# Kernel optimization log

Measured on AMD Instinct MI355X. Metric: run time of the kernel, lower is better.

Reference implementation:

```python
import jax, jax.numpy as jnp
import numpy as np

B, S, D, H = 2, 2048, 1024, 16
DH = D // H  # 64
SCALE = DH ** -0.5


def setup_inputs() -> dict:
    key = jax.random.key(0)
    ks = jax.random.split(key, 6)
    std = D ** -0.5
    return {
        "Q": jax.random.normal(ks[0], (B, S, D), jnp.float32),
        "prev": jax.random.normal(ks[1], (B, H, S, S), jnp.float32),
        "W_qkv": jax.random.normal(ks[2], (D, 3 * D), jnp.float32) * std,
        "b_qkv": jax.random.normal(ks[3], (3 * D,), jnp.float32) * 0.01,
        "W_out": jax.random.normal(ks[4], (D, D), jnp.float32) * std,
        "b_out": jax.random.normal(ks[5], (D,), jnp.float32) * 0.01,
    }


def reference(Q, prev, W_qkv, b_qkv, W_out, b_out):
    # fused QKV projection: [B,S,3D]
    qkv = jnp.einsum("bsd,de->bse", Q, W_qkv) + b_qkv
    # [B,S,H,3*DH] then split into q,k,v each [B,S,H,DH]
    qkv = qkv.reshape(B, S, H, 3 * DH)
    q, k, v = jnp.split(qkv, 3, axis=-1)
    # scores [B,H,S,S] with residual attention add
    scores = jnp.einsum("bqhd,bkhd->bhqk", q, k) * SCALE + prev
    attn = jax.nn.softmax(scores, axis=-1)  # dropout p=0.0 -> identity
    # context [B,S,H,DH] -> [B,S,D]
    context = jnp.einsum("bhqk,bkhd->bqhd", attn, v).reshape(B, S, D)
    output = jnp.einsum("bsd,de->bse", context, W_out) + b_out
    return output, scores
```

## Files before the change

kernel.cpp:

```cpp
#include <hip/hip_runtime.h>

typedef __attribute__((ext_vector_type(8))) short bf16x8;
typedef __attribute__((ext_vector_type(4))) float f32x4;
typedef __attribute__((ext_vector_type(4))) unsigned short u16x4;
typedef unsigned short ushort_t;
typedef unsigned int uint32;

constexpr int B_ = 2, S_ = 2048, D_ = 1024, H_ = 16, DH_ = 64;
constexpr int M_TOK = B_ * S_;
constexpr int N_QKV = 3 * D_;

#define DEV __device__ __forceinline__

DEV ushort_t f2bf(float f) {
  uint32 u = __builtin_bit_cast(uint32, f);
  u += 0x7fffu + ((u >> 16) & 1u);
  return (ushort_t)(u >> 16);
}

DEV float bf2f(ushort_t u) {
  uint32 x = ((uint32)u) << 16;
  return __builtin_bit_cast(float, x);
}

DEV void gll16(const void* g, void* l) {
  __builtin_amdgcn_global_load_lds(
      (const __attribute__((address_space(1))) void*)g,
      (__attribute__((address_space(3))) void*)l, 16, 0, 0);
}

__global__ __launch_bounds__(256) void k_cvt_q(const float* __restrict__ in,
                                               ushort_t* __restrict__ out) {
  int i = (blockIdx.x * 256 + threadIdx.x) * 4;
  float4 v = *(const float4*)(in + i);
  u16x4 o;
  o.x = f2bf(v.x); o.y = f2bf(v.y); o.z = f2bf(v.z); o.w = f2bf(v.w);
  *(u16x4*)(out + i) = o;
}

__global__ __launch_bounds__(256) void k_transpose_cvt(const float* __restrict__ in,
                                                       ushort_t* __restrict__ out,
                                                       int R, int C) {
  __shared__ float t[32][33];
  int bx = blockIdx.x, by = blockIdx.y;
  int tx = threadIdx.x & 31, ty = threadIdx.x >> 5;
#pragma unroll
  for (int i = 0; i < 4; ++i) {
    int r = by * 32 + ty + i * 8;
    t[ty + i * 8][tx] = in[(size_t)r * C + bx * 32 + tx];
  }
  __syncthreads();
#pragma unroll
  for (int i = 0; i < 4; ++i) {
    int orow = bx * 32 + ty + i * 8;
    int ocol = by * 32 + tx;
    out[(size_t)orow * R + ocol] = f2bf(t[tx][ty + i * 8]);
  }
}

__global__ __launch_bounds__(256) void k_gemm_qkv(
    const ushort_t* __restrict__ A,
    const ushort_t* __restrict__ Bt,
    const float* __restrict__ bias,
    ushort_t* __restrict__ qh,
    ushort_t* __restrict__ kh,
    ushort_t* __restrict__ vT) {
  constexpr int K = 1024;
  __shared__ ushort_t lA[128 * 32];
  __shared__ ushort_t lB[128 * 32];
  const int t = threadIdx.x, lane = t & 63, w = t >> 6;
  const int wm = w >> 1, wn = w & 1;
  const int bm = blockIdx.x & 31, bn = blockIdx.x >> 5;

  f32x4 acc[4][4];
#pragma unroll
  for (int i = 0; i < 4; ++i)
#pragma unroll
    for (int j = 0; j < 4; ++j) acc[i][j] = f32x4{0.f, 0.f, 0.f, 0.f};

  const int srow = t >> 2;
  const int scol = (t & 3) * 8;
  for (int k0 = 0; k0 < K; k0 += 32) {
    __syncthreads();
    gll16(A + (size_t)(bm * 128 + srow) * K + k0 + scol, lA + srow * 32 + scol);
    gll16(A + (size_t)(bm * 128 + 64 + srow) * K + k0 + scol, lA + (64 + srow) * 32 + scol);
    gll16(Bt + (size_t)(bn * 128 + srow) * K + k0 + scol, lB + srow * 32 + scol);
    gll16(Bt + (size_t)(bn * 128 + 64 + srow) * K + k0 + scol, lB + (64 + srow) * 32 + scol);
    asm volatile("s_waitcnt vmcnt(0)" ::: "memory");
    __syncthreads();
    bf16x8 af[4], bfr[4];
#pragma unroll
    for (int i = 0; i < 4; ++i)
      af[i] = *(const bf16x8*)(lA + (wm * 64 + i * 16 + (lane & 15)) * 32 + (lane >> 4) * 8);
#pragma unroll
    for (int j = 0; j < 4; ++j)
      bfr[j] = *(const bf16x8*)(lB + (wn * 64 + j * 16 + (lane & 15)) * 32 + (lane >> 4) * 8);
#pragma unroll
    for (int i = 0; i < 4; ++i)
#pragma unroll
      for (int j = 0; j < 4; ++j)
        acc[i][j] = __builtin_amdgcn_mfma_f32_16x16x32_bf16(af[i], bfr[j], acc[i][j], 0, 0, 0);
  }
#pragma unroll
  for (int i = 0; i < 4; ++i) {
#pragma unroll
    for (int j = 0; j < 4; ++j) {
#pragma unroll
      for (int p = 0; p < 4; ++p) {
        int row = bm * 128 + wm * 64 + i * 16 + (lane >> 4) * 4 + p;
        int col = bn * 128 + wn * 64 + j * 16 + (lane & 15);
        float v = acc[i][j][p] + bias[col];
        ushort_t bv = f2bf(v);
        int b = row >> 11, s = row & (S_ - 1);
        int h = col / 192, r = col - h * 192;
        size_t bh = (size_t)(b * H_ + h);
        if (r < 64)
          qh[(bh * S_ + s) * 64 + r] = bv;
        else if (r < 128)
          kh[(bh * S_ + s) * 64 + (r - 64)] = bv;
        else
          vT[(bh * 64 + (r - 128)) * S_ + s] = bv;
      }
    }
  }
}

__global__ __launch_bounds__(256, 2) void k_scores_pv(
    const ushort_t* __restrict__ qhp,
    const ushort_t* __restrict__ khp,
    const ushort_t* __restrict__ vT,
    const float* __restrict__ prev,
    float* __restrict__ scores,
    float* __restrict__ pstats,
    ushort_t* __restrict__ Opart) {
  __shared__ ushort_t lK[512 * 64];
  __shared__ ushort_t Plds[4][2048];
  const int t = threadIdx.x, lane = t & 63, w = t >> 6;
  int idx = (int)blockIdx.x;
  idx = (idx & 7) * 512 + (idx >> 3);
  const int rt = idx & 31, ct = (idx >> 5) & 3, bh = idx >> 7;
  const int row0 = rt * 64 + w * 16;
  const int kt0 = ct * 512;
  const int lo = lane & 15, hi = lane >> 4;

  const ushort_t* qb = qhp + ((size_t)bh * S_ + row0) * 64;
  const ushort_t* kb = khp + ((size_t)bh * S_ + kt0) * 64;
  const ushort_t* vb = vT + (size_t)bh * 64 * S_ + kt0;
  const float* pb = prev + (size_t)bh * S_ * S_ + (size_t)(row0 + lo) * S_ + kt0;
  float* sb = scores + (size_t)bh * S_ * S_ + (size_t)(row0 + lo) * S_ + kt0;

  bf16x8 qf0 = *(const bf16x8*)(qb + lo * 64 + hi * 8);
  bf16x8 qf1 = *(const bf16x8*)(qb + lo * 64 + 32 + hi * 8);

#pragma unroll
  for (int i = 0; i < 16; ++i) {
    int u = i * 256 + t;
    int r = u >> 3;
    int s = (u & 7) * 16;
    int cb = s ^ ((r & 7) << 4);
    gll16(kb + (size_t)r * 64 + cb / 2, (ushort_t*)lK + u * 8);
  }
  float4 pcur[8];
#pragma unroll
  for (int kf = 0; kf < 8; ++kf)
    pcur[kf] = *(const float4*)(pb + kf * 16 + hi * 4);
  asm volatile("s_waitcnt vmcnt(0)" ::: "memory");
  __syncthreads();

  const int swz = (lo & 7) << 4;
  const char* lkb = (const char*)lK;
  char* pw = (char*)&Plds[w][0];

  f32x4 acco[4];
#pragma unroll
  for (int dn = 0; dn < 4; ++dn) acco[dn] = f32x4{0.f, 0.f, 0.f, 0.f};
  float m_run = -1e30f, l_run = 0.f;

  for (int c = 0; c < 4; ++c) {
    bf16x8 vf[4][4];
#pragma unroll
    for (int kc = 0; kc < 4; ++kc)
#pragma unroll
      for (int dn = 0; dn < 4; ++dn)
        vf[kc][dn] = *(const bf16x8*)(vb + (size_t)(dn * 16 + lo) * S_ +
                                      c * 128 + kc * 32 + hi * 8);
    float4 pnext[8];
    if (c < 3) {
#pragma unroll
      for (int kf = 0; kf < 8; ++kf)
        pnext[kf] = *(const float4*)(pb + (c + 1) * 128 + kf * 16 + hi * 4);
    }
    f32x4 acc[8];
#pragma unroll
    for (int kf = 0; kf < 8; ++kf) acc[kf] = f32x4{0.f, 0.f, 0.f, 0.f};
#pragma unroll
    for (int kf = 0; kf < 8; ++kf) {
      int krow = c * 128 + kf * 16 + lo;
      bf16x8 k0 = *(const bf16x8*)(lkb + krow * 128 + ((hi * 16) ^ swz));
      bf16x8 k1 = *(const bf16x8*)(lkb + krow * 128 + ((64 + hi * 16) ^ swz));
      acc[kf] = __builtin_amdgcn_mfma_f32_16x16x32_bf16(k0, qf0, acc[kf], 0, 0, 0);
      acc[kf] = __builtin_amdgcn_mfma_f32_16x16x32_bf16(k1, qf1, acc[kf], 0, 0, 0);
    }
    float tmax = -1e30f;
#pragma unroll
    for (int kf = 0; kf < 8; ++kf) {
      acc[kf][0] = acc[kf][0] * 0.125f + pcur[kf].x;
      acc[kf][1] = acc[kf][1] * 0.125f + pcur[kf].y;
      acc[kf][2] = acc[kf][2] * 0.125f + pcur[kf].z;
      acc[kf][3] = acc[kf][3] * 0.125f + pcur[kf].w;
      __builtin_nontemporal_store(acc[kf], (f32x4*)(sb + c * 128 + kf * 16 + hi * 4));
      tmax = fmaxf(tmax, fmaxf(fmaxf(acc[kf][0], acc[kf][1]), fmaxf(acc[kf][2], acc[kf][3])));
    }
    tmax = fmaxf(tmax, __shfl_xor(tmax, 16));
    tmax = fmaxf(tmax, __shfl_xor(tmax, 32));
    float m_new = fmaxf(m_run, tmax);
    float fs = __expf(m_run - m_new);
    float lsum = 0.f;
#pragma unroll
    for (int kf = 0; kf < 8; ++kf) {
      float e0 = __expf(acc[kf][0] - m_new);
      float e1 = __expf(acc[kf][1] - m_new);
      float e2 = __expf(acc[kf][2] - m_new);
      float e3 = __expf(acc[kf][3] - m_new);
      lsum += (e0 + e1) + (e2 + e3);
      u16x4 pk;
      pk.x = f2bf(e0); pk.y = f2bf(e1); pk.z = f2bf(e2); pk.w = f2bf(e3);
      int byte = (lo * 256 + kf * 32 + hi * 8) ^ swz;
      *(u16x4*)(pw + byte) = pk;
    }
    lsum += __shfl_xor(lsum, 16);
    lsum += __shfl_xor(lsum, 32);
    m_run = m_new;
    l_run = l_run * fs + lsum;
#pragma unroll
    for (int dn = 0; dn < 4; ++dn)
#pragma unroll
      for (int p = 0; p < 4; ++p) acco[dn][p] *= fs;
#pragma unroll
    for (int kc = 0; kc < 4; ++kc) {
      int byte = (lo * 256 + kc * 64 + hi * 16) ^ swz;
      bf16x8 pa = *(const bf16x8*)(pw + byte);
#pragma unroll
      for (int dn = 0; dn < 4; ++dn)
        acco[dn] = __builtin_amdgcn_mfma_f32_16x16x32_bf16(vf[kc][dn], pa, acco[dn], 0, 0, 0);
    }
    if (c < 3) {
#pragma unroll
      for (int kf = 0; kf < 8; ++kf) pcur[kf] = pnext[kf];
    }
  }
  ushort_t* ob = Opart + (((size_t)bh * S_ + row0 + lo) * 4 + ct) * 64;
#pragma unroll
  for (int dn = 0; dn < 4; ++dn) {
    u16x4 ov;
#pragma unroll
    for (int p = 0; p < 4; ++p) ov[p] = f2bf(acco[dn][p]);
    *(u16x4*)(ob + dn * 16 + hi * 4) = ov;
  }
  if (hi == 0)
    *(float2*)(pstats + (((size_t)bh * S_ + row0 + lo) * 4 + ct) * 2) =
        float2{m_run, l_run};
}

__global__ __launch_bounds__(256) void k_combine(
    const float* __restrict__ pstats,
    const ushort_t* __restrict__ Opart,
    ushort_t* __restrict__ ctx) {
  const int t = threadIdx.x;
  const int row = blockIdx.x * 64 + (t >> 2);
  const int hi4 = t & 3;
  const int bh = row >> 11, s = row & (S_ - 1);

  const float* ps = pstats + (size_t)row * 8;
  float2 st[4];
#pragma unroll
  for (int i = 0; i < 4; ++i) st[i] = *(const float2*)(ps + i * 2);
  float m = fmaxf(fmaxf(st[0].x, st[1].x), fmaxf(st[2].x, st[3].x));
  float den = 0.f;
#pragma unroll
  for (int i = 0; i < 4; ++i) den += st[i].y * __expf(st[i].x - m);
  float sc[4];
#pragma unroll
  for (int i = 0; i < 4; ++i) sc[i] = __expf(st[i].x - m) / den;

  const ushort_t* ob = Opart + (size_t)row * 256 + hi4 * 16;
  float o[16];
#pragma unroll
  for (int j = 0; j < 16; ++j) o[j] = 0.f;
#pragma unroll
  for (int i = 0; i < 4; ++i) {
    bf16x8 a0 = *(const bf16x8*)(ob + i * 64);
    bf16x8 a1 = *(const bf16x8*)(ob + i * 64 + 8);
#pragma unroll
    for (int j = 0; j < 8; ++j) {
      o[j]     += bf2f((ushort_t)a0[j]) * sc[i];
      o[8 + j] += bf2f((ushort_t)a1[j]) * sc[i];
    }
  }
  const int b = bh >> 4, h = bh & 15;
  ushort_t* cp = ctx + (size_t)(b * S_ + s) * D_ + h * 64 + hi4 * 16;
#pragma unroll
  for (int g = 0; g < 4; ++g) {
    u16x4 ov;
#pragma unroll
    for (int p = 0; p < 4; ++p) ov[p] = f2bf(o[g * 4 + p]);
    *(u16x4*)(cp + g * 4) = ov;
  }
}

__global__ __launch_bounds__(256) void k_gemm_out(
    const ushort_t* __restrict__ A,
    const ushort_t* __restrict__ Bt,
    const float* __restrict__ bias,
    float* __restrict__ out) {
  constexpr int K = 1024;
  __shared__ ushort_t lA[128 * 32];
  __shared__ ushort_t lB[128 * 32];
  const int t = threadIdx.x, lane = t & 63, w = t >> 6;
  const int wm = w >> 1, wn = w & 1;
  const int bm = blockIdx.x & 31, bn = blockIdx.x >> 5;

  f32x4 acc[4][4];
#pragma unroll
  for (int i = 0; i < 4; ++i)
#pragma unroll
    for (int j = 0; j < 4; ++j) acc[i][j] = f32x4{0.f, 0.f, 0.f, 0.f};

  const int srow = t >> 2;
  const int scol = (t & 3) * 8;
  for (int k0 = 0; k0 < K; k0 += 32) {
    __syncthreads();
    gll16(A + (size_t)(bm * 128 + srow) * K + k0 + scol, lA + srow * 32 + scol);
    gll16(A + (size_t)(bm * 128 + 64 + srow) * K + k0 + scol, lA + (64 + srow) * 32 + scol);
    gll16(Bt + (size_t)(bn * 128 + srow) * K + k0 + scol, lB + srow * 32 + scol);
    gll16(Bt + (size_t)(bn * 128 + 64 + srow) * K + k0 + scol, lB + (64 + srow) * 32 + scol);
    asm volatile("s_waitcnt vmcnt(0)" ::: "memory");
    __syncthreads();
    bf16x8 af[4], bfr[4];
#pragma unroll
    for (int i = 0; i < 4; ++i)
      af[i] = *(const bf16x8*)(lA + (wm * 64 + i * 16 + (lane & 15)) * 32 + (lane >> 4) * 8);
#pragma unroll
    for (int j = 0; j < 4; ++j)
      bfr[j] = *(const bf16x8*)(lB + (wn * 64 + j * 16 + (lane & 15)) * 32 + (lane >> 4) * 8);
#pragma unroll
    for (int i = 0; i < 4; ++i)
#pragma unroll
      for (int j = 0; j < 4; ++j)
        acc[i][j] = __builtin_amdgcn_mfma_f32_16x16x32_bf16(af[i], bfr[j], acc[i][j], 0, 0, 0);
  }
#pragma unroll
  for (int i = 0; i < 4; ++i) {
#pragma unroll
    for (int j = 0; j < 4; ++j) {
#pragma unroll
      for (int p = 0; p < 4; ++p) {
        int row = bm * 128 + wm * 64 + i * 16 + (lane >> 4) * 4 + p;
        int col = bn * 128 + wn * 64 + j * 16 + (lane & 15);
        out[(size_t)row * 1024 + col] = acc[i][j][p] + bias[col];
      }
    }
  }
}

extern "C" void kernel_launch(void* const* d_in, const int* in_sizes, int n_in,
                              void* d_out, int out_size, void* d_ws, size_t ws_size,
                              hipStream_t stream) {
  (void)in_sizes; (void)n_in; (void)out_size; (void)ws_size;
  const float* Q     = (const float*)d_in[0];
  const float* prev  = (const float*)d_in[1];
  const float* W_qkv = (const float*)d_in[2];
  const float* b_qkv = (const float*)d_in[3];
  const float* W_out = (const float*)d_in[4];
  const float* b_out = (const float*)d_in[5];
  float* out = (float*)d_out;
  float* scores_out = out + (size_t)M_TOK * D_;

  char* ws = (char*)d_ws;
  ushort_t* Qb    = (ushort_t*)(ws + (size_t)0);
  ushort_t* WqkvT = (ushort_t*)(ws + ((size_t)8  << 20));
  ushort_t* WoutT = (ushort_t*)(ws + ((size_t)14 << 20));
  ushort_t* qh    = (ushort_t*)(ws + ((size_t)16 << 20));
  ushort_t* kh    = (ushort_t*)(ws + ((size_t)24 << 20));
  ushort_t* vT    = (ushort_t*)(ws + ((size_t)32 << 20));
  ushort_t* ctx   = (ushort_t*)(ws + ((size_t)40 << 20));
  ushort_t* Opart = (ushort_t*)(ws + ((size_t)48 << 20));
  float*    pstats = (float*)Qb;

  k_cvt_q<<<4096, 256, 0, stream>>>(Q, Qb);
  k_transpose_cvt<<<dim3(96, 32), 256, 0, stream>>>(W_qkv, WqkvT, 1024, 3072);
  k_transpose_cvt<<<dim3(32, 32), 256, 0, stream>>>(W_out, WoutT, 1024, 1024);
  k_gemm_qkv<<<768, 256, 0, stream>>>(Qb, WqkvT, b_qkv, qh, kh, vT);
  k_scores_pv<<<4096, 256, 0, stream>>>(qh, kh, vT, prev, scores_out, pstats, Opart);
  k_combine<<<1024, 256, 0, stream>>>(pstats, Opart, ctx);
  k_gemm_out<<<256, 256, 0, stream>>>(ctx, WoutT, b_out, out);
}
```

Measured before the change: 423.9 us.

## Make scores kernel persistent over eight row tiles to reuse LDS K tile

Each block of the scores/PV kernel now handles eight consecutive 64-row tiles for one (head, 512-column) slice instead of one, so the K slice staged in LDS is reused eight times and the grid drops from 4096 to 512 blocks. The next tile's Q fragments and first prev chunk are prefetched during the last chunk of the current tile through ping-ponged registers. The scores store changes from nontemporal to a plain store. The cost is fewer blocks (512 on a large GPU with two blocks per CU allowed), so latency hiding and load balance may suffer, and register pressure rises.

```diff
diff --git a/kernel.cpp b/kernel.cpp
--- a/kernel.cpp
+++ b/kernel.cpp
@@ -137,20 +137,16 @@
   __shared__ ushort_t Plds[4][2048];
   const int t = threadIdx.x, lane = t & 63, w = t >> 6;
   int idx = (int)blockIdx.x;
-  idx = (idx & 7) * 512 + (idx >> 3);
-  const int rt = idx & 31, ct = (idx >> 5) & 3, bh = idx >> 7;
-  const int row0 = rt * 64 + w * 16;
+  idx = (idx & 7) * 64 + (idx >> 3);
+  const int bh = idx >> 4, ct = (idx >> 2) & 3, rtg = idx & 3;
   const int kt0 = ct * 512;
   const int lo = lane & 15, hi = lane >> 4;
 
-  const ushort_t* qb = qhp + ((size_t)bh * S_ + row0) * 64;
+  const ushort_t* qbase = qhp + (size_t)bh * S_ * 64;
   const ushort_t* kb = khp + ((size_t)bh * S_ + kt0) * 64;
   const ushort_t* vb = vT + (size_t)bh * 64 * S_ + kt0;
-  const float* pb = prev + (size_t)bh * S_ * S_ + (size_t)(row0 + lo) * S_ + kt0;
-  float* sb = scores + (size_t)bh * S_ * S_ + (size_t)(row0 + lo) * S_ + kt0;
-
-  bf16x8 qf0 = *(const bf16x8*)(qb + lo * 64 + hi * 8);
-  bf16x8 qf1 = *(const bf16x8*)(qb + lo * 64 + 32 + hi * 8);
+  const float* prev_base = prev + (size_t)bh * S_ * S_ + kt0;
+  float* scores_base = scores + (size_t)bh * S_ * S_ + kt0;
 
 #pragma unroll
   for (int i = 0; i < 16; ++i) {
@@ -160,10 +156,14 @@
     int cb = s ^ ((r & 7) << 4);
     gll16(kb + (size_t)r * 64 + cb / 2, (ushort_t*)lK + u * 8);
   }
+  const int row00 = rtg * 512 + w * 16;
+  bf16x8 qfA0 = *(const bf16x8*)(qbase + (row00 + lo) * 64 + hi * 8);
+  bf16x8 qfA1 = *(const bf16x8*)(qbase + (row00 + lo) * 64 + 32 + hi * 8);
+  bf16x8 qfB0, qfB1;
   float4 pcur[8];
 #pragma unroll
   for (int kf = 0; kf < 8; ++kf)
-    pcur[kf] = *(const float4*)(pb + kf * 16 + hi * 4);
+    pcur[kf] = *(const float4*)(prev_base + (size_t)(row00 + lo) * S_ + kf * 16 + hi * 4);
   asm volatile("s_waitcnt vmcnt(0)" ::: "memory");
   __syncthreads();
 
@@ -171,95 +171,105 @@
   const char* lkb = (const char*)lK;
   char* pw = (char*)&Plds[w][0];
 
-  f32x4 acco[4];
-#pragma unroll
-  for (int dn = 0; dn < 4; ++dn) acco[dn] = f32x4{0.f, 0.f, 0.f, 0.f};
-  float m_run = -1e30f, l_run = 0.f;
-
-  for (int c = 0; c < 4; ++c) {
-    bf16x8 vf[4][4];
-#pragma unroll
-    for (int kc = 0; kc < 4; ++kc)
-#pragma unroll
-      for (int dn = 0; dn < 4; ++dn)
-        vf[kc][dn] = *(const bf16x8*)(vb + (size_t)(dn * 16 + lo) * S_ +
-                                      c * 128 + kc * 32 + hi * 8);
-    float4 pnext[8];
-    if (c < 3) {
-#pragma unroll
-      for (int kf = 0; kf < 8; ++kf)
-        pnext[kf] = *(const float4*)(pb + (c + 1) * 128 + kf * 16 + hi * 4);
-    }
-    f32x4 acc[8];
-#pragma unroll
-    for (int kf = 0; kf < 8; ++kf) acc[kf] = f32x4{0.f, 0.f, 0.f, 0.f};
-#pragma unroll
-    for (int kf = 0; kf < 8; ++kf) {
-      int krow = c * 128 + kf * 16 + lo;
-      bf16x8 k0 = *(const bf16x8*)(lkb + krow * 128 + ((hi * 16) ^ swz));
-      bf16x8 k1 = *(const bf16x8*)(lkb + krow * 128 + ((64 + hi * 16) ^ swz));
-      acc[kf] = __builtin_amdgcn_mfma_f32_16x16x32_bf16(k0, qf0, acc[kf], 0, 0, 0);
-      acc[kf] = __builtin_amdgcn_mfma_f32_16x16x32_bf16(k1, qf1, acc[kf], 0, 0, 0);
-    }
-    float tmax = -1e30f;
-#pragma unroll
-    for (int kf = 0; kf < 8; ++kf) {
-      acc[kf][0] = acc[kf][0] * 0.125f + pcur[kf].x;
-      acc[kf][1] = acc[kf][1] * 0.125f + pcur[kf].y;
-      acc[kf][2] = acc[kf][2] * 0.125f + pcur[kf].z;
-      acc[kf][3] = acc[kf][3] * 0.125f + pcur[kf].w;
-      __builtin_nontemporal_store(acc[kf], (f32x4*)(sb + c * 128 + kf * 16 + hi * 4));
-      tmax = fmaxf(tmax, fmaxf(fmaxf(acc[kf][0], acc[kf][1]), fmaxf(acc[kf][2], acc[kf][3])));
-    }
-    tmax = fmaxf(tmax, __shfl_xor(tmax, 16));
-    tmax = fmaxf(tmax, __shfl_xor(tmax, 32));
-    float m_new = fmaxf(m_run, tmax);
-    float fs = __expf(m_run - m_new);
-    float lsum = 0.f;
-#pragma unroll
-    for (int kf = 0; kf < 8; ++kf) {
-      float e0 = __expf(acc[kf][0] - m_new);
-      float e1 = __expf(acc[kf][1] - m_new);
-      float e2 = __expf(acc[kf][2] - m_new);
-      float e3 = __expf(acc[kf][3] - m_new);
-      lsum += (e0 + e1) + (e2 + e3);
-      u16x4 pk;
-      pk.x = f2bf(e0); pk.y = f2bf(e1); pk.z = f2bf(e2); pk.w = f2bf(e3);
-      int byte = (lo * 256 + kf * 32 + hi * 8) ^ swz;
-      *(u16x4*)(pw + byte) = pk;
-    }
-    lsum += __shfl_xor(lsum, 16);
-    lsum += __shfl_xor(lsum, 32);
-    m_run = m_new;
-    l_run = l_run * fs + lsum;
-#pragma unroll
-    for (int dn = 0; dn < 4; ++dn)
-#pragma unroll
-      for (int p = 0; p < 4; ++p) acco[dn][p] *= fs;
-#pragma unroll
-    for (int kc = 0; kc < 4; ++kc) {
-      int byte = (lo * 256 + kc * 64 + hi * 16) ^ swz;
-      bf16x8 pa = *(const bf16x8*)(pw + byte);
-#pragma unroll
-      for (int dn = 0; dn < 4; ++dn)
-        acco[dn] = __builtin_amdgcn_mfma_f32_16x16x32_bf16(vf[kc][dn], pa, acco[dn], 0, 0, 0);
-    }
-    if (c < 3) {
-#pragma unroll
-      for (int kf = 0; kf < 8; ++kf) pcur[kf] = pnext[kf];
-    }
-  }
-  ushort_t* ob = Opart + (((size_t)bh * S_ + row0 + lo) * 4 + ct) * 64;
-#pragma unroll
-  for (int dn = 0; dn < 4; ++dn) {
-    u16x4 ov;
-#pragma unroll
-    for (int p = 0; p < 4; ++p) ov[p] = f2bf(acco[dn][p]);
-    *(u16x4*)(ob + dn * 16 + hi * 4) = ov;
-  }
-  if (hi == 0)
-    *(float2*)(pstats + (((size_t)bh * S_ + row0 + lo) * 4 + ct) * 2) =
-        float2{m_run, l_run};
+#define RT_BODY(QF0, QF1, NQF0, NQF1, RT, LAST)                               \
+  {                                                                           \
+    const int row0 = rtg * 512 + (RT) * 64 + w * 16;                          \
+    const float* pb = prev_base + (size_t)(row0 + lo) * S_;                   \
+    float* sb = scores_base + (size_t)(row0 + lo) * S_;                       \
+    f32x4 acco[4];                                                            \
+    _Pragma("unroll") for (int dn = 0; dn < 4; ++dn)                          \
+        acco[dn] = f32x4{0.f, 0.f, 0.f, 0.f};                                 \
+    float m_run = -1e30f, l_run = 0.f;                                        \
+    _Pragma("unroll") for (int c = 0; c < 4; ++c) {                           \
+      bf16x8 vf[4][4];                                                        \
+      _Pragma("unroll") for (int kc = 0; kc < 4; ++kc)                        \
+          _Pragma("unroll") for (int dn = 0; dn < 4; ++dn)                    \
+              vf[kc][dn] = *(const bf16x8*)(vb + (size_t)(dn * 16 + lo) * S_ +\
+                                            c * 128 + kc * 32 + hi * 8);      \
+      if (c == 3 && !(LAST)) {       \
+        NQF0 = *(const bf16x8*)(qbase + (row0 + 64 + lo) * 64 + hi * 8);      \
+        NQF1 = *(const bf16x8*)(qbase + (row0 + 64 + lo) * 64 + 32 + hi * 8); \
+      }                                                                       \
+      float4 pnext[8];                                                        \
+      if (c < 3) {                                                            \
+        _Pragma("unroll") for (int kf = 0; kf < 8; ++kf)                      \
+            pnext[kf] = *(const float4*)(pb + (c + 1) * 128 + kf * 16 + hi * 4);\
+      } else if (!(LAST)) {                                                   \
+        _Pragma("unroll") for (int kf = 0; kf < 8; ++kf)                      \
+            pnext[kf] = *(const float4*)(pb + 64 * S_ + kf * 16 + hi * 4);    \
+      }                                                                       \
+      f32x4 acc[8];                                                           \
+      _Pragma("unroll") for (int kf = 0; kf < 8; ++kf)                        \
+          acc[kf] = f32x4{0.f, 0.f, 0.f, 0.f};                                \
+      _Pragma("unroll") for (int kf = 0; kf < 8; ++kf) {                      \
+        int krow = c * 128 + kf * 16 + lo;                                    \
+        bf16x8 k0 = *(const bf16x8*)(lkb + krow * 128 + ((hi * 16) ^ swz));   \
+        bf16x8 k1 = *(const bf16x8*)(lkb + krow * 128 + ((64 + hi * 16) ^ swz));\
+        acc[kf] = __builtin_amdgcn_mfma_f32_16x16x32_bf16(k0, QF0, acc[kf], 0, 0, 0);\
+        acc[kf] = __builtin_amdgcn_mfma_f32_16x16x32_bf16(k1, QF1, acc[kf], 0, 0, 0);\
+      }                                                                       \
+      float tmax = -1e30f;                                                    \
+      _Pragma("unroll") for (int kf = 0; kf < 8; ++kf) {                      \
+        acc[kf][0] = acc[kf][0] * 0.125f + pcur[kf].x;                        \
+        acc[kf][1] = acc[kf][1] * 0.125f + pcur[kf].y;                        \
+        acc[kf][2] = acc[kf][2] * 0.125f + pcur[kf].z;                        \
+        acc[kf][3] = acc[kf][3] * 0.125f + pcur[kf].w;                        \
+        *(float4*)(sb + c * 128 + kf * 16 + hi * 4) =                         \
+            float4{acc[kf][0], acc[kf][1], acc[kf][2], acc[kf][3]};           \
+        tmax = fmaxf(tmax, fmaxf(fmaxf(acc[kf][0], acc[kf][1]),               \
+                                 fmaxf(acc[kf][2], acc[kf][3])));             \
+      }                                                                       \
+      tmax = fmaxf(tmax, __shfl_xor(tmax, 16));                               \
+      tmax = fmaxf(tmax, __shfl_xor(tmax, 32));                               \
+      float m_new = fmaxf(m_run, tmax);                                       \
+      float fs = __expf(m_run - m_new);                                       \
+      float lsum = 0.f;                                                       \
+      _Pragma("unroll") for (int kf = 0; kf < 8; ++kf) {                      \
+        float e0 = __expf(acc[kf][0] - m_new);                                \
+        float e1 = __expf(acc[kf][1] - m_new);                                \
+        float e2 = __expf(acc[kf][2] - m_new);                                \
+        float e3 = __expf(acc[kf][3] - m_new);                                \
+        lsum += (e0 + e1) + (e2 + e3);                                        \
+        u16x4 pk;                                                             \
+        pk.x = f2bf(e0); pk.y = f2bf(e1); pk.z = f2bf(e2); pk.w = f2bf(e3);   \
+        int byte = (lo * 256 + kf * 32 + hi * 8) ^ swz;                       \
+        *(u16x4*)(pw + byte) = pk;                                            \
+      }                                                                       \
+      lsum += __shfl_xor(lsum, 16);                                           \
+      lsum += __shfl_xor(lsum, 32);                                           \
+      m_run = m_new;                                                          \
+      l_run = l_run * fs + lsum;                                              \
+      _Pragma("unroll") for (int dn = 0; dn < 4; ++dn)                        \
+          _Pragma("unroll") for (int p = 0; p < 4; ++p) acco[dn][p] *= fs;    \
+      _Pragma("unroll") for (int kc = 0; kc < 4; ++kc) {                      \
+        int byte = (lo * 256 + kc * 64 + hi * 16) ^ swz;                      \
+        bf16x8 pa = *(const bf16x8*)(pw + byte);                              \
+        _Pragma("unroll") for (int dn = 0; dn < 4; ++dn)                      \
+            acco[dn] = __builtin_amdgcn_mfma_f32_16x16x32_bf16(               \
+                vf[kc][dn], pa, acco[dn], 0, 0, 0);                           \
+      }                                                                       \
+      if (c < 3 || !(LAST)) {                                                 \
+        _Pragma("unroll") for (int kf = 0; kf < 8; ++kf) pcur[kf] = pnext[kf];\
+      }                                                                       \
+    }                                                                         \
+    ushort_t* ob = Opart + (((size_t)bh * S_ + row0 + lo) * 4 + ct) * 64;     \
+    _Pragma("unroll") for (int dn = 0; dn < 4; ++dn) {                        \
+      u16x4 ov;                                                               \
+      _Pragma("unroll") for (int p = 0; p < 4; ++p) ov[p] = f2bf(acco[dn][p]);\
+      *(u16x4*)(ob + dn * 16 + hi * 4) = ov;                                  \
+    }                                                                         \
+    if (hi == 0)                                                              \
+      *(float2*)(pstats + (((size_t)bh * S_ + row0 + lo) * 4 + ct) * 2) =     \
+          float2{m_run, l_run};                                               \
+  }
+
+  for (int i = 0; i < 3; ++i) {
+    RT_BODY(qfA0, qfA1, qfB0, qfB1, 2 * i, false);
+    RT_BODY(qfB0, qfB1, qfA0, qfA1, 2 * i + 1, false);
+  }
+  RT_BODY(qfA0, qfA1, qfB0, qfB1, 6, false);
+  RT_BODY(qfB0, qfB1, qfA0, qfA1, 7, true);
+#undef RT_BODY
 }
 
 __global__ __launch_bounds__(256) void k_combine(
@@ -391,7 +401,7 @@
   k_transpose_cvt<<<dim3(96, 32), 256, 0, stream>>>(W_qkv, WqkvT, 1024, 3072);
   k_transpose_cvt<<<dim3(32, 32), 256, 0, stream>>>(W_out, WoutT, 1024, 1024);
   k_gemm_qkv<<<768, 256, 0, stream>>>(Qb, WqkvT, b_qkv, qh, kh, vT);
-  k_scores_pv<<<4096, 256, 0, stream>>>(qh, kh, vT, prev, scores_out, pstats, Opart);
+  k_scores_pv<<<512, 256, 0, stream>>>(qh, kh, vT, prev, scores_out, pstats, Opart);
   k_combine<<<1024, 256, 0, stream>>>(pstats, Opart, ctx);
   k_gemm_out<<<256, 256, 0, stream>>>(ctx, WoutT, b_out, out);
 }
```

Measured after the change: 546.3 us. 1.29x slower.
